# Optimization experiments

Measured on AMD Instinct MI355X. Metric: run time of the kernel, lower is better.

Reference implementation:

```python
import jax, jax.numpy as jnp
import numpy as np

L, D, H, T_MAX, V = 6, 1024, 16, 1024, 50257
HD = D // H
EPS = 1e-5


def setup_inputs() -> dict:
    key = jax.random.key(0)
    ks = jax.random.split(key, 12)
    s = 0.02
    return {
        "idx": jax.random.randint(ks[0], (2, 1024), 0, V, dtype=jnp.int32),
        "tok_W": jax.random.normal(ks[1], (V, D), jnp.float32) * s,
        "pos_W": jax.random.normal(ks[2], (T_MAX, D), jnp.float32) * s,
        "ln1_g": jnp.ones((L, D), jnp.float32),
        "ln1_b": jnp.zeros((L, D), jnp.float32),
        "Wq": jax.random.normal(ks[3], (L, D, D), jnp.float32) * s,
        "Wk": jax.random.normal(ks[4], (L, D, D), jnp.float32) * s,
        "Wv": jax.random.normal(ks[5], (L, D, D), jnp.float32) * s,
        "Wo": jax.random.normal(ks[6], (L, D, D), jnp.float32) * s,
        "bo": jnp.zeros((L, D), jnp.float32),
        "ln2_g": jnp.ones((L, D), jnp.float32),
        "ln2_b": jnp.zeros((L, D), jnp.float32),
        "W1": jax.random.normal(ks[7], (L, D, 4 * D), jnp.float32) * s,
        "b1": jnp.zeros((L, 4 * D), jnp.float32),
        "W2": jax.random.normal(ks[8], (L, 4 * D, D), jnp.float32) * s,
        "b2": jnp.zeros((L, D), jnp.float32),
        "lnf_g": jnp.ones((D,), jnp.float32),
        "lnf_b": jnp.zeros((D,), jnp.float32),
    }


def _ln(x, g, b):
    mu = jnp.mean(x, axis=-1, keepdims=True)
    var = jnp.mean(jnp.square(x - mu), axis=-1, keepdims=True)
    return (x - mu) * jax.lax.rsqrt(var + EPS) * g + b


def reference(idx, tok_W, pos_W, ln1_g, ln1_b, Wq, Wk, Wv, Wo, bo,
              ln2_g, ln2_b, W1, b1, W2, b2, lnf_g, lnf_b):
    B, T = idx.shape
    x = tok_W[idx] + pos_W[:T]  # [B,T,D]
    mask = jnp.tril(jnp.ones((T, T), bool))

    def block(x, p):
        (g1, b1n, wq, wk, wv, wo, bob, g2, b2n, w1, bb1, w2, bb2) = p
        h = _ln(x, g1, b1n)
        q = (h @ wq).reshape(B, T, H, HD)
        k = (h @ wk).reshape(B, T, H, HD)
        v = (h @ wv).reshape(B, T, H, HD)
        scores = jnp.einsum('bqhd,bkhd->bhqk', q, k) * (HD ** -0.5)
        scores = jnp.where(mask, scores, -jnp.inf)
        wei = jax.nn.softmax(scores, axis=-1)
        att = jnp.einsum('bhqk,bkhd->bqhd', wei, v).reshape(B, T, D)
        x = x + att @ wo + bob
        h2 = _ln(x, g2, b2n)
        ff = jax.nn.gelu(h2 @ w1 + bb1, approximate=False) @ w2 + bb2
        return x + ff, None

    params = (ln1_g, ln1_b, Wq, Wk, Wv, Wo, bo, ln2_g, ln2_b, W1, b1, W2, b2)
    x, _ = jax.lax.scan(block, x, params)
    x = _ln(x, lnf_g, lnf_b)
    logits = x @ tok_W.T  # weight-tied lm_head
    return logits
```

## Files before the change

### kernel.cpp

```cpp
#include <hip/hip_runtime.h>
#include <hip/hip_bf16.h>
#include <math.h>


using u16 = unsigned short;
typedef __attribute__((ext_vector_type(4))) float f32x4;
typedef __attribute__((ext_vector_type(8))) short s16x8;

static __device__ __forceinline__ u16 f2b(float f) {
    __hip_bfloat16 h = __float2bfloat16(f);
    return *reinterpret_cast<u16*>(&h);
}
static __device__ __forceinline__ float b2f(u16 u) {
    __hip_bfloat16 h = *reinterpret_cast<__hip_bfloat16*>(&u);
    return __bfloat162float(h);
}

#define GLDS16(gp, lp) __builtin_amdgcn_global_load_lds( \
    (const __attribute__((address_space(1))) unsigned int*)(gp), \
    (__attribute__((address_space(3))) unsigned int*)(lp), 16, 0, 0)

__global__ __launch_bounds__(256) void gemm_bt(
    const u16* __restrict__ A, const u16* __restrict__ Bt,
    float* __restrict__ Cf, u16* __restrict__ Cb,
    const float* __restrict__ bias, const float* __restrict__ resid,
    int M, int N, int K, int lda, int ldb, int ldc,
    long long aO, long long aI, long long bO, long long bI,
    long long cO, long long cI, int ZH, float scale, int flags)
{
    __shared__ u16 As[128 * 32];
    __shared__ u16 Bs[128 * 32];

    const int t = threadIdx.x;
    const int lane = t & 63, wave = t >> 6;
    const int wm = wave >> 1, wn = wave & 1;
    const int lr = lane & 15, lq = lane >> 4;
    const int m0 = blockIdx.x * 128;
    const int n0 = blockIdx.y * 128;
    const int zb = blockIdx.z / ZH, zh = blockIdx.z % ZH;
    const long long offA = (long long)zb * aO + (long long)zh * aI;
    const long long offB = (long long)zb * bO + (long long)zh * bI;
    const long long offC = (long long)zb * cO + (long long)zh * cI;

    f32x4 acc[4][4];
#pragma unroll
    for (int i = 0; i < 4; i++)
#pragma unroll
        for (int j = 0; j < 4; j++) acc[i][j] = (f32x4){0.f, 0.f, 0.f, 0.f};

    const int r0 = t >> 2;
    const int kk0 = (t & 3) << 3;
    const int wvb = wave << 10;

    for (int k0 = 0; k0 < K; k0 += 32) {
        __syncthreads();
        {
            const u16* ap = A + offA + (size_t)(m0 + r0) * lda + (k0 + kk0);
            GLDS16(ap, (char*)As + wvb);
            GLDS16(ap + (size_t)64 * lda, (char*)As + 4096 + wvb);
        }
        {
            int nr  = n0 + r0;      if (nr  >= N) nr  = N - 1;
            int nr2 = n0 + r0 + 64; if (nr2 >= N) nr2 = N - 1;
            const u16* bp  = Bt + offB + (size_t)nr  * ldb + (k0 + kk0);
            const u16* bp2 = Bt + offB + (size_t)nr2 * ldb + (k0 + kk0);
            GLDS16(bp,  (char*)Bs + wvb);
            GLDS16(bp2, (char*)Bs + 4096 + wvb);
        }
        __syncthreads();

        s16x8 a[4], b[4];
#pragma unroll
        for (int i = 0; i < 4; i++)
            a[i] = *(const s16x8*)&As[(wm * 64 + i * 16 + lr) * 32 + lq * 8];
#pragma unroll
        for (int j = 0; j < 4; j++)
            b[j] = *(const s16x8*)&Bs[(wn * 64 + j * 16 + lr) * 32 + lq * 8];
#pragma unroll
        for (int i = 0; i < 4; i++)
#pragma unroll
            for (int j = 0; j < 4; j++)
                acc[i][j] = __builtin_amdgcn_mfma_f32_16x16x32_bf16(
                    a[i], b[j], acc[i][j], 0, 0, 0);
    }

    const bool obf = (flags & 1) != 0;
    const bool gel = (flags & 2) != 0;
#pragma unroll
    for (int i = 0; i < 4; i++) {
#pragma unroll
        for (int j = 0; j < 4; j++) {
            int col = n0 + wn * 64 + j * 16 + lr;
            if (col >= N) continue;
#pragma unroll
            for (int r = 0; r < 4; r++) {
                int row = m0 + wm * 64 + i * 16 + lq * 4 + r;
                float v = acc[i][j][r] * scale;
                if (bias) v += bias[col];
                if (gel) v = 0.5f * v * (1.f + erff(v * 0.70710678118f));
                long long ci = offC + (long long)row * ldc + col;
                if (resid) v += resid[ci];
                if (obf) Cb[ci] = f2b(v);
                else     Cf[ci] = v;
            }
        }
    }
}

__global__ __launch_bounds__(256) void transpose_conv(
    const void* __restrict__ in, u16* __restrict__ out,
    int R, int C, int ldi, int ldo, long long zi, long long zo, int in_bf16)
{
    __shared__ float tile[32][33];
    int tx = threadIdx.x & 31, ty = threadIdx.x >> 5;
    int r0 = blockIdx.y * 32, c0 = blockIdx.x * 32;
    long long ioff = (long long)blockIdx.z * zi;
    long long ooff = (long long)blockIdx.z * zo;
#pragma unroll
    for (int i = 0; i < 32; i += 8) {
        long long r = r0 + ty + i, c = c0 + tx;
        float v;
        if (in_bf16) v = b2f(((const u16*)in)[ioff + r * ldi + c]);
        else         v = ((const float*)in)[ioff + r * ldi + c];
        tile[ty + i][tx] = v;
    }
    __syncthreads();
#pragma unroll
    for (int i = 0; i < 32; i += 8) {
        long long c = c0 + ty + i, r = r0 + tx;
        out[ooff + c * ldo + r] = f2b(tile[tx][ty + i]);
    }
}

__global__ __launch_bounds__(256) void conv_f2b(
    const float* __restrict__ in, u16* __restrict__ out, size_t n)
{
    size_t i = ((size_t)blockIdx.x * 256 + threadIdx.x) * 4;
    if (i >= n) return;
    float4 f = *(const float4*)&in[i];
    out[i + 0] = f2b(f.x);
    out[i + 1] = f2b(f.y);
    out[i + 2] = f2b(f.z);
    out[i + 3] = f2b(f.w);
}

__global__ __launch_bounds__(256) void embed_k(
    const int* __restrict__ idx, const float* __restrict__ tokW,
    const float* __restrict__ posW, float* __restrict__ x)
{
    int row = blockIdx.x;
    int tt = row & 1023;
    int tok = idx[row];
    int c = threadIdx.x * 4;
    float4 a = *(const float4*)&tokW[(size_t)tok * 1024 + c];
    float4 p = *(const float4*)&posW[(size_t)tt * 1024 + c];
    float4 r = {a.x + p.x, a.y + p.y, a.z + p.z, a.w + p.w};
    *(float4*)&x[(size_t)row * 1024 + c] = r;
}

__global__ __launch_bounds__(256) void ln_k(
    const float* __restrict__ x, const float* __restrict__ g,
    const float* __restrict__ b, u16* __restrict__ out)
{
    __shared__ float sbuf[8];
    int row = blockIdx.x;
    int c = threadIdx.x * 4;
    float4 v = *(const float4*)&x[(size_t)row * 1024 + c];
    float s = v.x + v.y + v.z + v.w;
    float s2 = v.x * v.x + v.y * v.y + v.z * v.z + v.w * v.w;
#pragma unroll
    for (int o = 32; o > 0; o >>= 1) {
        s += __shfl_down(s, o, 64);
        s2 += __shfl_down(s2, o, 64);
    }
    int lane = threadIdx.x & 63, wave = threadIdx.x >> 6;
    if (lane == 0) { sbuf[wave] = s; sbuf[4 + wave] = s2; }
    __syncthreads();
    float mean = (sbuf[0] + sbuf[1] + sbuf[2] + sbuf[3]) * (1.f / 1024.f);
    float m2 = (sbuf[4] + sbuf[5] + sbuf[6] + sbuf[7]) * (1.f / 1024.f);
    float rstd = rsqrtf(m2 - mean * mean + 1e-5f);
    float vals[4] = {v.x, v.y, v.z, v.w};
    u16 o4[4];
#pragma unroll
    for (int i = 0; i < 4; i++) {
        float y = (vals[i] - mean) * rstd * g[c + i] + b[c + i];
        o4[i] = f2b(y);
    }
    *(uint2*)&out[(size_t)row * 1024 + c] = *(uint2*)o4;
}

__global__ __launch_bounds__(256) void softmax_causal(u16* __restrict__ S)
{
    __shared__ float sbuf[8];
    int row = blockIdx.x;
    int q = row & 1023;
    u16* p = S + (size_t)row * 1024;
    int c = threadIdx.x * 4;
    u16 u4[4];
    *(uint2*)u4 = *(const uint2*)&p[c];
    float v[4];
#pragma unroll
    for (int i = 0; i < 4; i++) v[i] = (c + i <= q) ? b2f(u4[i]) : -1e30f;
    float mx = fmaxf(fmaxf(v[0], v[1]), fmaxf(v[2], v[3]));
#pragma unroll
    for (int o = 32; o > 0; o >>= 1) mx = fmaxf(mx, __shfl_down(mx, o, 64));
    int lane = threadIdx.x & 63, wave = threadIdx.x >> 6;
    if (lane == 0) sbuf[wave] = mx;
    __syncthreads();
    mx = fmaxf(fmaxf(sbuf[0], sbuf[1]), fmaxf(sbuf[2], sbuf[3]));
    float e[4], sum = 0.f;
#pragma unroll
    for (int i = 0; i < 4; i++) {
        e[i] = (c + i <= q) ? expf(v[i] - mx) : 0.f;
        sum += e[i];
    }
#pragma unroll
    for (int o = 32; o > 0; o >>= 1) sum += __shfl_down(sum, o, 64);
    if (lane == 0) sbuf[4 + wave] = sum;
    __syncthreads();
    float inv = 1.f / (sbuf[4] + sbuf[5] + sbuf[6] + sbuf[7]);
#pragma unroll
    for (int i = 0; i < 4; i++) u4[i] = f2b(e[i] * inv);
    *(uint2*)&p[c] = *(uint2*)u4;
}

extern "C" void kernel_launch(void* const* d_in, const int* in_sizes, int n_in,
                              void* d_out, int out_size, void* d_ws, size_t ws_size,
                              hipStream_t stream)
{
    const int*   idx  = (const int*)d_in[0];
    const float* tokW = (const float*)d_in[1];
    const float* posW = (const float*)d_in[2];
    const float* ln1g = (const float*)d_in[3];
    const float* ln1b = (const float*)d_in[4];
    const float* Wq   = (const float*)d_in[5];
    const float* Wk   = (const float*)d_in[6];
    const float* Wv   = (const float*)d_in[7];
    const float* Wo   = (const float*)d_in[8];
    const float* bo   = (const float*)d_in[9];
    const float* ln2g = (const float*)d_in[10];
    const float* ln2b = (const float*)d_in[11];
    const float* W1   = (const float*)d_in[12];
    const float* b1   = (const float*)d_in[13];
    const float* W2   = (const float*)d_in[14];
    const float* b2   = (const float*)d_in[15];
    const float* lnfg = (const float*)d_in[16];
    const float* lnfb = (const float*)d_in[17];
    float* out = (float*)d_out;

    char* w = (char*)d_ws;
    auto alloc = [&](size_t bytes) -> char* {
        char* p = w;
        w += (bytes + 255) & ~(size_t)255;
        return p;
    };
    float* x    = (float*)alloc(2048ull * 1024 * 4);
    u16* h      = (u16*)alloc(2048ull * 1024 * 2);
    u16* qkv    = (u16*)alloc(2048ull * 3072 * 2);
    u16* vt     = (u16*)alloc(2ull * 1024 * 1024 * 2);
    u16* attb   = (u16*)alloc(2048ull * 1024 * 2);
    u16* ffb    = (u16*)alloc(2048ull * 4096 * 2);
    u16* wqkvT  = (u16*)alloc(3072ull * 1024 * 2);
    u16* woT    = (u16*)alloc(1024ull * 1024 * 2);
    u16* w1T    = (u16*)alloc(4096ull * 1024 * 2);
    u16* w2T    = (u16*)alloc(1024ull * 4096 * 2);
    u16* S      = (u16*)alloc(50257ull * 1024 * 2);
    u16* twb    = S;

    auto gemm = [&](const u16* A, const u16* Bt, float* Cf, u16* Cb,
                    const float* bias, const float* resid,
                    int M, int N, int K, int lda, int ldb, int ldc,
                    long long aO, long long aI, long long bO, long long bI,
                    long long cO, long long cI, int Z, int ZH,
                    float scale, int flags) {
        dim3 g(M / 128, (N + 127) / 128, Z);
        gemm_bt<<<g, dim3(256), 0, stream>>>(A, Bt, Cf, Cb, bias, resid,
                                             M, N, K, lda, ldb, ldc,
                                             aO, aI, bO, bI, cO, cI,
                                             ZH, scale, flags);
    };

    embed_k<<<2048, 256, 0, stream>>>(idx, tokW, posW, x);

    const long long TT = 1024ll * 1024;
    for (int l = 0; l < 6; l++) {
        const float* wq = Wq + (size_t)l * 1024 * 1024;
        const float* wk = Wk + (size_t)l * 1024 * 1024;
        const float* wv = Wv + (size_t)l * 1024 * 1024;
        const float* wo = Wo + (size_t)l * 1024 * 1024;
        const float* w1 = W1 + (size_t)l * 1024 * 4096;
        const float* w2 = W2 + (size_t)l * 4096 * 1024;

        dim3 tg(32, 32, 1);
        transpose_conv<<<tg, 256, 0, stream>>>(wq, wqkvT,            1024, 1024, 1024, 1024, 0, 0, 0);
        transpose_conv<<<tg, 256, 0, stream>>>(wk, wqkvT + 1048576,  1024, 1024, 1024, 1024, 0, 0, 0);
        transpose_conv<<<tg, 256, 0, stream>>>(wv, wqkvT + 2097152,  1024, 1024, 1024, 1024, 0, 0, 0);
        transpose_conv<<<tg, 256, 0, stream>>>(wo, woT,              1024, 1024, 1024, 1024, 0, 0, 0);
        transpose_conv<<<dim3(128, 32, 1), 256, 0, stream>>>(w1, w1T, 1024, 4096, 4096, 1024, 0, 0, 0);
        transpose_conv<<<dim3(32, 128, 1), 256, 0, stream>>>(w2, w2T, 4096, 1024, 1024, 4096, 0, 0, 0);

        ln_k<<<2048, 256, 0, stream>>>(x, ln1g + l * 1024, ln1b + l * 1024, h);
        gemm(h, wqkvT, nullptr, qkv, nullptr, nullptr,
             2048, 3072, 1024, 1024, 1024, 3072,
             0, 0, 0, 0, 0, 0, 1, 1, 1.f, 1);
        transpose_conv<<<dim3(32, 32, 2), 256, 0, stream>>>(
            qkv + 2048, vt, 1024, 1024, 3072, 1024,
            1024ll * 3072, TT, 1);
        gemm(qkv, qkv + 1024, nullptr, S, nullptr, nullptr,
             1024, 1024, 64, 3072, 3072, 1024,
             1024ll * 3072, 64, 1024ll * 3072, 64, 16 * TT, TT,
             32, 16, 0.125f, 1);
        softmax_causal<<<32768, 256, 0, stream>>>(S);
        gemm(S, vt, nullptr, attb, nullptr, nullptr,
             1024, 64, 1024, 1024, 1024, 1024,
             16 * TT, TT, TT, 64ll * 1024, TT, 64,
             32, 16, 1.f, 1);
        gemm(attb, woT, x, nullptr, bo + l * 1024, x,
             2048, 1024, 1024, 1024, 1024, 1024,
             0, 0, 0, 0, 0, 0, 1, 1, 1.f, 0);
        ln_k<<<2048, 256, 0, stream>>>(x, ln2g + l * 1024, ln2b + l * 1024, h);
        gemm(h, w1T, nullptr, ffb, b1 + l * 4096, nullptr,
             2048, 4096, 1024, 1024, 1024, 4096,
             0, 0, 0, 0, 0, 0, 1, 1, 1.f, 1 | 2);
        gemm(ffb, w2T, x, nullptr, b2 + l * 1024, x,
             2048, 1024, 4096, 4096, 4096, 1024,
             0, 0, 0, 0, 0, 0, 1, 1, 1.f, 0);
    }

    ln_k<<<2048, 256, 0, stream>>>(x, lnfg, lnfb, h);
    conv_f2b<<<50257, 256, 0, stream>>>(tokW, twb, 50257ull * 1024);
    gemm(h, twb, out, nullptr, nullptr, nullptr,
         2048, 50257, 1024, 1024, 1024, 50257,
         0, 0, 0, 0, 0, 0, 1, 1, 1.f, 0);
}
```

Measured before the change: 3.293 ms.

## Pair attention heads in PV GEMM, swizzle blocks across XCDs, hoist load pointers

The P·V GEMM previously launched with N=64, so half of each 128-wide tile's B columns and MFMA work were wasted on clamped rows. It now processes two heads per block: a dualA flag loads two heads' score matrices into a doubled A shared buffer, and each wave-column uses its own head's A. All GEMMs also remap block IDs so consecutive tiles land on the same XCD for L2 locality, and global pointers are hoisted out of the k-loop and incremented. The cost is extra LDS per block, which may lower occupancy, plus an XCD remap that assumes 8 XCDs.

```diff
diff --git a/kernel.cpp b/kernel.cpp
--- a/kernel.cpp
+++ b/kernel.cpp
@@ -28,17 +28,28 @@
     long long aO, long long aI, long long bO, long long bI,
     long long cO, long long cI, int ZH, float scale, int flags)
 {
-    __shared__ u16 As[128 * 32];
+    __shared__ u16 As[2 * 128 * 32];
     __shared__ u16 Bs[128 * 32];
 
     const int t = threadIdx.x;
     const int lane = t & 63, wave = t >> 6;
     const int wm = wave >> 1, wn = wave & 1;
     const int lr = lane & 15, lq = lane >> 4;
-    const int m0 = blockIdx.x * 128;
-    const int n0 = blockIdx.y * 128;
+
+    const int gx = gridDim.x;
+    const int nwg = gx * gridDim.y;
+    const int orig = blockIdx.y * gx + blockIdx.x;
+    const int qn = nwg >> 3, rn = nwg & 7;
+    const int xcd = orig & 7, loc = orig >> 3;
+    const int nid = (xcd < rn ? xcd * (qn + 1)
+                              : rn * (qn + 1) + (xcd - rn) * qn) + loc;
+    const int m0 = (nid % gx) * 128;
+    const int n0 = (nid / gx) * 128;
+
+    const bool dualA = (flags & 4) != 0;
     const int zb = blockIdx.z / ZH, zh = blockIdx.z % ZH;
-    const long long offA = (long long)zb * aO + (long long)zh * aI;
+    const long long offA = (long long)zb * aO
+                         + (long long)(dualA ? 2 * zh : zh) * aI;
     const long long offB = (long long)zb * bO + (long long)zh * bI;
     const long long offC = (long long)zb * cO + (long long)zh * cI;
 
@@ -52,27 +63,31 @@
     const int kk0 = (t & 3) << 3;
     const int wvb = wave << 10;
 
+    const u16* ap = A + offA + (size_t)(m0 + r0) * lda + kk0;
+    const u16* apB = dualA ? (ap + aI) : ap;
+    int nr  = n0 + r0;      if (nr  >= N) nr  = N - 1;
+    int nr2 = n0 + r0 + 64; if (nr2 >= N) nr2 = N - 1;
+    const u16* bp  = Bt + offB + (size_t)nr  * ldb + kk0;
+    const u16* bp2 = Bt + offB + (size_t)nr2 * ldb + kk0;
+
+    const u16* Asw = As + (dualA ? (wn * (128 * 32)) : 0);
+
     for (int k0 = 0; k0 < K; k0 += 32) {
         __syncthreads();
-        {
-            const u16* ap = A + offA + (size_t)(m0 + r0) * lda + (k0 + kk0);
-            GLDS16(ap, (char*)As + wvb);
-            GLDS16(ap + (size_t)64 * lda, (char*)As + 4096 + wvb);
+        GLDS16(ap,                      (char*)As + wvb);
+        GLDS16(ap + (size_t)64 * lda,   (char*)As + 4096 + wvb);
+        if (dualA) {
+            GLDS16(apB,                    (char*)As + 8192 + wvb);
+            GLDS16(apB + (size_t)64 * lda, (char*)As + 12288 + wvb);
         }
-        {
-            int nr  = n0 + r0;      if (nr  >= N) nr  = N - 1;
-            int nr2 = n0 + r0 + 64; if (nr2 >= N) nr2 = N - 1;
-            const u16* bp  = Bt + offB + (size_t)nr  * ldb + (k0 + kk0);
-            const u16* bp2 = Bt + offB + (size_t)nr2 * ldb + (k0 + kk0);
-            GLDS16(bp,  (char*)Bs + wvb);
-            GLDS16(bp2, (char*)Bs + 4096 + wvb);
-        }
+        GLDS16(bp,  (char*)Bs + wvb);
+        GLDS16(bp2, (char*)Bs + 4096 + wvb);
         __syncthreads();
 
         s16x8 a[4], b[4];
 #pragma unroll
         for (int i = 0; i < 4; i++)
-            a[i] = *(const s16x8*)&As[(wm * 64 + i * 16 + lr) * 32 + lq * 8];
+            a[i] = *(const s16x8*)&Asw[(wm * 64 + i * 16 + lr) * 32 + lq * 8];
 #pragma unroll
         for (int j = 0; j < 4; j++)
             b[j] = *(const s16x8*)&Bs[(wn * 64 + j * 16 + lr) * 32 + lq * 8];
@@ -82,6 +97,8 @@
             for (int j = 0; j < 4; j++)
                 acc[i][j] = __builtin_amdgcn_mfma_f32_16x16x32_bf16(
                     a[i], b[j], acc[i][j], 0, 0, 0);
+
+        ap += 32; apB += 32; bp += 32; bp2 += 32;
     }
 
     const bool obf = (flags & 1) != 0;
@@ -312,9 +329,9 @@
              32, 16, 0.125f, 1);
         softmax_causal<<<32768, 256, 0, stream>>>(S);
         gemm(S, vt, nullptr, attb, nullptr, nullptr,
-             1024, 64, 1024, 1024, 1024, 1024,
-             16 * TT, TT, TT, 64ll * 1024, TT, 64,
-             32, 16, 1.f, 1);
+             1024, 128, 1024, 1024, 1024, 1024,
+             16 * TT, TT, TT, 128ll * 1024, TT, 128,
+             16, 8, 1.f, 1 | 4);
         gemm(attb, woT, x, nullptr, bo + l * 1024, x,
              2048, 1024, 1024, 1024, 1024, 1024,
              0, 0, 0, 0, 0, 0, 1, 1, 1.f, 0);
```

Result: faster. 3.155 ms (-4.2%).
